# Performance work log

Hardware: AMD Instinct MI355X
Metric: run time of the kernel (lower is better)

## Reference

```python
import jax, jax.numpy as jnp
import numpy as np

NEURONS = 4096
K = 512

def setup_inputs() -> dict:
    key = jax.random.key(0)
    s = jax.random.normal(key, (16384, NEURONS), dtype=jnp.float32)
    return {"s": s}

def reference(s) -> jnp.ndarray:
    # Original: sort each row ascending, zero the smallest (neurons - k) entries,
    # i.e. keep only the k largest values per row. With continuous random inputs
    # (no ties) this equals thresholding at the k-th largest value per row.
    topk_vals, _ = jax.lax.top_k(s, K)          # [B, K], descending
    thresh = topk_vals[:, -1:]                   # k-th largest per row, [B, 1]
    return jnp.where(s >= thresh, s, jnp.zeros((), dtype=s.dtype))
```

## Files before the change

kernel.cpp:

```cpp
#include <hip/hip_runtime.h>

#define ROWS 16384
#define COLS 4096
#define KSEL 512
#define WAVES_PER_BLOCK 4
#define THREADS (WAVES_PER_BLOCK * 64)
#define NCOPY 4
#define HSTRIDE 260

__device__ __forceinline__ unsigned map_f(float f) {
    unsigned u = __float_as_uint(f);
    return u ^ (0x80000000u | (unsigned)((int)u >> 31));
}
__device__ __forceinline__ float unmap_f(unsigned m) {
    return __uint_as_float(m ^ (0x80000000u | ~(unsigned)((int)m >> 31)));
}

__global__ __launch_bounds__(THREADS, 4) void kwta_kernel(const float* __restrict__ in,
                                                          float* __restrict__ out) {
    __shared__ __align__(16) unsigned histmem[WAVES_PER_BLOCK][NCOPY * HSTRIDE];

    const int lane = threadIdx.x & 63;
    const int wave = threadIdx.x >> 6;
    const int row  = blockIdx.x * WAVES_PER_BLOCK + wave;
    unsigned* h = histmem[wave];
    const int copy = (lane & 3) * HSTRIDE;

    const float4* __restrict__ inrow  = (const float4*)(in  + (size_t)row * COLS);
    float4*       __restrict__ outrow = (float4*)(out + (size_t)row * COLS);

    unsigned v[64];
#pragma unroll
    for (int i = 0; i < 16; i++) {
        float4 f = inrow[lane + 64 * i];
        v[4 * i + 0] = map_f(f.x);
        v[4 * i + 1] = map_f(f.y);
        v[4 * i + 2] = map_f(f.z);
        v[4 * i + 3] = map_f(f.w);
    }

    unsigned prefix = 0;
    unsigned kk = KSEL;

#pragma unroll
    for (int pass = 0; pass < 4; pass++) {
        const int shift = 24 - 8 * pass;

        uint4 z = make_uint4(0u, 0u, 0u, 0u);
#pragma unroll
        for (int i = 0; i < 5; i++) {
            int w4 = lane + 64 * i;
            if (w4 < (NCOPY * HSTRIDE) / 4) ((uint4*)h)[w4] = z;
        }

        if (pass == 0) {
#pragma unroll
            for (int i = 0; i < 64; i++)
                atomicAdd(&h[copy + (v[i] >> 24)], 1u);
        } else {
            const int hs = shift + 8;
#pragma unroll
            for (int i = 0; i < 64; i++) {
                if (((v[i] ^ prefix) >> hs) == 0u)
                    atomicAdd(&h[copy + ((v[i] >> shift) & 255u)], 1u);
            }
        }

        uint4 c0 = ((const uint4*)(h + 0 * HSTRIDE))[lane];
        uint4 c1 = ((const uint4*)(h + 1 * HSTRIDE))[lane];
        uint4 c2 = ((const uint4*)(h + 2 * HSTRIDE))[lane];
        uint4 c3 = ((const uint4*)(h + 3 * HSTRIDE))[lane];
        unsigned n0 = c0.x + c1.x + c2.x + c3.x;
        unsigned n1 = c0.y + c1.y + c2.y + c3.y;
        unsigned n2 = c0.z + c1.z + c2.z + c3.z;
        unsigned n3 = c0.w + c1.w + c2.w + c3.w;

        unsigned ls3 = n3, ls2 = n3 + n2, ls1 = ls2 + n1, tot = ls1 + n0;

        unsigned S = tot;
#pragma unroll
        for (int off = 1; off < 64; off <<= 1) {
            unsigned o = __shfl(S, lane + off);
            S += (lane + off < 64) ? o : 0u;
        }
        const unsigned R = S - tot;

        const unsigned S3 = R + ls3, S2 = R + ls2, S1 = R + ls1, S0 = R + tot;
        unsigned dig = 0, nk = 0;
        bool found = false;
        if (S3 >= kk && R  < kk) { dig = 4 * lane + 3; nk = kk - R;  found = true; }
        if (S2 >= kk && S3 < kk) { dig = 4 * lane + 2; nk = kk - S3; found = true; }
        if (S1 >= kk && S2 < kk) { dig = 4 * lane + 1; nk = kk - S2; found = true; }
        if (S0 >= kk && S1 < kk) { dig = 4 * lane + 0; nk = kk - S1; found = true; }

        unsigned long long m = __ballot(found);
        int src = (int)__ffsll((unsigned long long)m) - 1;
        dig = __shfl(dig, src);
        nk  = __shfl(nk, src);

        prefix |= dig << shift;
        kk = nk;
    }

#pragma unroll
    for (int i = 0; i < 16; i++) {
        float4 o;
        o.x = (v[4 * i + 0] >= prefix) ? unmap_f(v[4 * i + 0]) : 0.0f;
        o.y = (v[4 * i + 1] >= prefix) ? unmap_f(v[4 * i + 1]) : 0.0f;
        o.z = (v[4 * i + 2] >= prefix) ? unmap_f(v[4 * i + 2]) : 0.0f;
        o.w = (v[4 * i + 3] >= prefix) ? unmap_f(v[4 * i + 3]) : 0.0f;
        outrow[lane + 64 * i] = o;
    }
}

extern "C" void kernel_launch(void* const* d_in, const int* in_sizes, int n_in,
                              void* d_out, int out_size, void* d_ws, size_t ws_size,
                              hipStream_t stream) {
    const float* s = (const float*)d_in[0];
    float* out = (float*)d_out;
    kwta_kernel<<<ROWS / WAVES_PER_BLOCK, THREADS, 0, stream>>>(s, out);
}
```

Before: 441.6 us.

## Process one row per block with shared histograms instead of one row per wave

Each 256-thread block now handles one row, so every thread holds 16 values instead of 64 and register pressure falls, allowing higher occupancy (launch bounds 8). Histograms are shared block-wide: 8 replicated copies for the first pass, then a separate pre-zeroed histogram per later pass, which removes the per-pass zeroing at the cost of __syncthreads barriers. Every wave redundantly computes the digit selection from the shared counts. The risk is atomic contention on the shared histograms and barrier overhead.

```diff
diff --git a/kernel.cpp b/kernel.cpp
--- a/kernel.cpp
+++ b/kernel.cpp
@@ -3,9 +3,8 @@
 #define ROWS 16384
 #define COLS 4096
 #define KSEL 512
-#define WAVES_PER_BLOCK 4
-#define THREADS (WAVES_PER_BLOCK * 64)
-#define NCOPY 4
+#define THREADS 256
+#define NCOPY0 8
 #define HSTRIDE 260
 
 __device__ __forceinline__ unsigned map_f(float f) {
@@ -16,100 +15,101 @@
     return __uint_as_float(m ^ (0x80000000u | ~(unsigned)((int)m >> 31)));
 }
 
-__global__ __launch_bounds__(THREADS, 4) void kwta_kernel(const float* __restrict__ in,
+__device__ __forceinline__ void select_digit(unsigned n0, unsigned n1, unsigned n2,
+                                             unsigned n3, int lane, int shift,
+                                             unsigned& prefix, unsigned& kk) {
+    unsigned ls3 = n3, ls2 = n3 + n2, ls1 = ls2 + n1, tot = ls1 + n0;
+    unsigned S = tot;
+#pragma unroll
+    for (int off = 1; off < 64; off <<= 1) {
+        unsigned o = __shfl(S, lane + off);
+        S += (lane + off < 64) ? o : 0u;
+    }
+    const unsigned R = S - tot;
+    const unsigned S3 = R + ls3, S2 = R + ls2, S1 = R + ls1, S0 = R + tot;
+    unsigned dig = 0, nk = 0;
+    bool found = false;
+    if (S3 >= kk && R  < kk) { dig = 4 * lane + 3; nk = kk - R;  found = true; }
+    if (S2 >= kk && S3 < kk) { dig = 4 * lane + 2; nk = kk - S3; found = true; }
+    if (S1 >= kk && S2 < kk) { dig = 4 * lane + 1; nk = kk - S2; found = true; }
+    if (S0 >= kk && S1 < kk) { dig = 4 * lane + 0; nk = kk - S1; found = true; }
+    unsigned long long m = __ballot(found);
+    int src = (int)__ffsll(m) - 1;
+    prefix |= (unsigned)__shfl(dig, src) << shift;
+    kk = (unsigned)__shfl(nk, src);
+}
+
+__global__ __launch_bounds__(THREADS, 8) void kwta_kernel(const float* __restrict__ in,
                                                           float* __restrict__ out) {
-    __shared__ __align__(16) unsigned histmem[WAVES_PER_BLOCK][NCOPY * HSTRIDE];
+    __shared__ __align__(16) unsigned hist[(NCOPY0 + 3) * HSTRIDE];
 
-    const int lane = threadIdx.x & 63;
-    const int wave = threadIdx.x >> 6;
-    const int row  = blockIdx.x * WAVES_PER_BLOCK + wave;
-    unsigned* h = histmem[wave];
-    const int copy = (lane & 3) * HSTRIDE;
+    const int tid  = threadIdx.x;
+    const int lane = tid & 63;
+    const int row  = blockIdx.x;
 
     const float4* __restrict__ inrow  = (const float4*)(in  + (size_t)row * COLS);
     float4*       __restrict__ outrow = (float4*)(out + (size_t)row * COLS);
 
-    unsigned v[64];
+    unsigned v[16];
 #pragma unroll
-    for (int i = 0; i < 16; i++) {
-        float4 f = inrow[lane + 64 * i];
+    for (int i = 0; i < 4; i++) {
+        float4 f = inrow[tid + THREADS * i];
         v[4 * i + 0] = map_f(f.x);
         v[4 * i + 1] = map_f(f.y);
         v[4 * i + 2] = map_f(f.z);
         v[4 * i + 3] = map_f(f.w);
     }
 
+    {
+        const uint4 z = make_uint4(0u, 0u, 0u, 0u);
+#pragma unroll
+        for (int i = 0; i < 3; i++) {
+            int w4 = tid + THREADS * i;
+            if (w4 < (NCOPY0 + 3) * HSTRIDE / 4) ((uint4*)hist)[w4] = z;
+        }
+    }
+    __syncthreads();
+
     unsigned prefix = 0;
     unsigned kk = KSEL;
 
+    {
+        unsigned* h0 = hist + (tid & (NCOPY0 - 1)) * HSTRIDE;
 #pragma unroll
-    for (int pass = 0; pass < 4; pass++) {
-        const int shift = 24 - 8 * pass;
-
-        uint4 z = make_uint4(0u, 0u, 0u, 0u);
+        for (int i = 0; i < 16; i++) atomicAdd(&h0[v[i] >> 24], 1u);
+        __syncthreads();
+        unsigned n0 = 0, n1 = 0, n2 = 0, n3 = 0;
 #pragma unroll
-        for (int i = 0; i < 5; i++) {
-            int w4 = lane + 64 * i;
-            if (w4 < (NCOPY * HSTRIDE) / 4) ((uint4*)h)[w4] = z;
+        for (int c = 0; c < NCOPY0; c++) {
+            uint4 t = ((const uint4*)(hist + c * HSTRIDE))[lane];
+            n0 += t.x; n1 += t.y; n2 += t.z; n3 += t.w;
         }
-
-        if (pass == 0) {
-#pragma unroll
-            for (int i = 0; i < 64; i++)
-                atomicAdd(&h[copy + (v[i] >> 24)], 1u);
-        } else {
-            const int hs = shift + 8;
-#pragma unroll
-            for (int i = 0; i < 64; i++) {
-                if (((v[i] ^ prefix) >> hs) == 0u)
-                    atomicAdd(&h[copy + ((v[i] >> shift) & 255u)], 1u);
-            }
-        }
-
-        uint4 c0 = ((const uint4*)(h + 0 * HSTRIDE))[lane];
-        uint4 c1 = ((const uint4*)(h + 1 * HSTRIDE))[lane];
-        uint4 c2 = ((const uint4*)(h + 2 * HSTRIDE))[lane];
-        uint4 c3 = ((const uint4*)(h + 3 * HSTRIDE))[lane];
-        unsigned n0 = c0.x + c1.x + c2.x + c3.x;
-        unsigned n1 = c0.y + c1.y + c2.y + c3.y;
-        unsigned n2 = c0.z + c1.z + c2.z + c3.z;
-        unsigned n3 = c0.w + c1.w + c2.w + c3.w;
-
-        unsigned ls3 = n3, ls2 = n3 + n2, ls1 = ls2 + n1, tot = ls1 + n0;
-
-        unsigned S = tot;
-#pragma unroll
-        for (int off = 1; off < 64; off <<= 1) {
-            unsigned o = __shfl(S, lane + off);
-            S += (lane + off < 64) ? o : 0u;
-        }
-        const unsigned R = S - tot;
-
-        const unsigned S3 = R + ls3, S2 = R + ls2, S1 = R + ls1, S0 = R + tot;
-        unsigned dig = 0, nk = 0;
-        bool found = false;
-        if (S3 >= kk && R  < kk) { dig = 4 * lane + 3; nk = kk - R;  found = true; }
-        if (S2 >= kk && S3 < kk) { dig = 4 * lane + 2; nk = kk - S3; found = true; }
-        if (S1 >= kk && S2 < kk) { dig = 4 * lane + 1; nk = kk - S2; found = true; }
-        if (S0 >= kk && S1 < kk) { dig = 4 * lane + 0; nk = kk - S1; found = true; }
-
-        unsigned long long m = __ballot(found);
-        int src = (int)__ffsll((unsigned long long)m) - 1;
-        dig = __shfl(dig, src);
-        nk  = __shfl(nk, src);
-
-        prefix |= dig << shift;
-        kk = nk;
+        select_digit(n0, n1, n2, n3, lane, 24, prefix, kk);
     }
 
 #pragma unroll
-    for (int i = 0; i < 16; i++) {
+    for (int pass = 1; pass < 4; pass++) {
+        const int shift = 24 - 8 * pass;
+        const int hs = shift + 8;
+        unsigned* hp = hist + (NCOPY0 + pass - 1) * HSTRIDE;
+#pragma unroll
+        for (int i = 0; i < 16; i++) {
+            if (((v[i] ^ prefix) >> hs) == 0u)
+                atomicAdd(&hp[(v[i] >> shift) & 255u], 1u);
+        }
+        __syncthreads();
+        uint4 t = ((const uint4*)hp)[lane];
+        select_digit(t.x, t.y, t.z, t.w, lane, shift, prefix, kk);
+    }
+
+#pragma unroll
+    for (int i = 0; i < 4; i++) {
         float4 o;
         o.x = (v[4 * i + 0] >= prefix) ? unmap_f(v[4 * i + 0]) : 0.0f;
         o.y = (v[4 * i + 1] >= prefix) ? unmap_f(v[4 * i + 1]) : 0.0f;
         o.z = (v[4 * i + 2] >= prefix) ? unmap_f(v[4 * i + 2]) : 0.0f;
         o.w = (v[4 * i + 3] >= prefix) ? unmap_f(v[4 * i + 3]) : 0.0f;
-        outrow[lane + 64 * i] = o;
+        outrow[tid + THREADS * i] = o;
     }
 }
 
@@ -118,5 +118,5 @@
                               hipStream_t stream) {
     const float* s = (const float*)d_in[0];
     float* out = (float*)d_out;
-    kwta_kernel<<<ROWS / WAVES_PER_BLOCK, THREADS, 0, stream>>>(s, out);
+    kwta_kernel<<<ROWS, THREADS, 0, stream>>>(s, out);
 }
```

Result: faster. 429.0 us (-2.9%).
